# Kernel optimization log

Measured on AMD Instinct MI355X. Metric: run time of the kernel, lower is better.

## Reference

```python
import jax, jax.numpy as jnp
import numpy as np


def setup_inputs() -> dict:
    key = jax.random.key(0)
    k1, k2 = jax.random.split(key)
    z = jax.random.normal(k1, (16, 256, 64, 64), dtype=jnp.float32)  # (t, latent_dim, H, W)
    emb = jax.random.normal(k2, (1024, 256), dtype=jnp.float32)      # (n_codes, latent_dim)
    return {"z": z, "emb": emb}


def reference(z, emb):
    # z: (t, a, b, c) with a == latent_dim; emb: (n_codes, a)
    t, a, b, c = z.shape
    # rearrange 't a b c -> t (b c) a'
    x = z.reshape(t, a, b * c).transpose(0, 2, 1)  # (t, bc, a)
    x2 = jnp.sum(x * x, axis=-1, keepdims=True)          # (t, bc, 1)
    e2 = jnp.sum(emb * emb, axis=-1)                     # (n_codes,)
    d2 = x2 + e2 - 2.0 * jnp.einsum('tna,ka->tnk', x, emb)  # (t, bc, n_codes)
    codes = jnp.argmin(d2, axis=-1)                      # (t, bc)
    return codes.reshape(t, b, c)
```

## Files before the change

### kernel.cpp

```cpp
#include <hip/hip_runtime.h>
#include <hip/hip_bf16.h>

#define TPB 512
#define NCODES 1024
#define DIMS 256
#define PIXB 64
#define DELTA 3.0f
#define CAP 16

typedef __attribute__((ext_vector_type(8))) short bf16x8;
typedef __attribute__((ext_vector_type(4))) float f32x4;

__device__ __forceinline__ void gll16(const void* g, void* l) {
    __builtin_amdgcn_global_load_lds(
        (const __attribute__((address_space(1))) void*)g,
        (__attribute__((address_space(3))) void*)l, 16, 0, 0);
}

__global__ __launch_bounds__(256) void prep_kernel(const float* __restrict__ emb,
                                                   ushort* __restrict__ eb,
                                                   float* __restrict__ e2) {
    const int w = threadIdx.x >> 6;
    const int l = threadIdx.x & 63;
    const int c = blockIdx.x * 4 + w;
    float4 v = *(const float4*)(emb + (size_t)c * DIMS + 4 * l);
    __hip_bfloat16 h0 = __float2bfloat16(v.x), h1 = __float2bfloat16(v.y);
    __hip_bfloat16 h2 = __float2bfloat16(v.z), h3 = __float2bfloat16(v.w);
    ushort4 u;
    u.x = *(ushort*)&h0; u.y = *(ushort*)&h1; u.z = *(ushort*)&h2; u.w = *(ushort*)&h3;
    const int st = (c >> 8) * 8 + (l >> 3);
    const int w8 = (c >> 5) & 7;
    const int cl = c & 31;
    const int j  = (l >> 1) & 3;
    const int e  = (4 * l) & 7;
    *(ushort4*)(eb + (((size_t)(st * 8 + w8) << 10) + (j << 8) + cl * 8 + e)) = u;
    float sq = v.x * v.x + v.y * v.y + v.z * v.z + v.w * v.w;
#pragma unroll
    for (int off = 1; off < 64; off <<= 1) sq += __shfl_xor(sq, off);
    if (l == 0) e2[c] = sq;
}

__global__ __launch_bounds__(TPB, 4) void vq_kernel(const float* __restrict__ z,
                                                    const float* __restrict__ emb,
                                                    const ushort* __restrict__ eb,
                                                    const float* __restrict__ e2g,
                                                    int* __restrict__ out) {
    __shared__ __align__(16) ushort xs2[32 * 64 * 8];
    __shared__ __align__(16) ushort es[2 * 8 * 1024];
    __shared__ float wmin[8 * 64];
    __shared__ float minval[64];
    __shared__ int   cnt[64];
    __shared__ int   cand[64 * CAP];
    __shared__ float scand[64 * CAP];

    const int tid = threadIdx.x;
    const int w   = tid >> 6;
    const int L   = tid & 63;
    const int col = L & 15;
    const int q   = L >> 4;
    const int pixbase = blockIdx.x * PIXB;
    const int t  = pixbase >> 12;
    const int n0 = pixbase & 4095;

#define STAGE(b, st) do {                                                         \
        const ushort* _src = eb + (((size_t)(st) * 8 + w) << 10) + (L << 3);      \
        ushort* _dst = &es[(((b) << 3) + w) * 1024];                              \
        gll16(_src,       _dst);                                                  \
        gll16(_src + 512, _dst + 512);                                            \
    } while (0)

    const float* zbase = z + (((size_t)t * DIMS) << 12) + n0;

#define STAGE_Z(r_, h_) do {                                                      \
        _Pragma("unroll")                                                         \
        for (int i = 0; i < 2; ++i) {                                             \
            const float* _src = zbase                                             \
                + ((size_t)((r_) * 64 + w * 8 + i * 4 + (L >> 4)) << 12)          \
                + ((L & 15) << 2);                                                \
            ushort* _dst = &es[(h_) * 8192 + (w * 2 + i) * 512];                  \
            gll16(_src, _dst);                                                    \
        }                                                                         \
    } while (0)

#define CONVERT(r_, h_) do {                                                      \
        const float* _zs = (const float*)&es[(h_) * 8192];                        \
        _Pragma("unroll")                                                         \
        for (int j = 0; j < 2; ++j) {                                             \
            const int _dl = w * 8 + j * 4;                                        \
            float _a0 = _zs[(_dl + 0) * 64 + L];                                  \
            float _a1 = _zs[(_dl + 1) * 64 + L];                                  \
            float _a2 = _zs[(_dl + 2) * 64 + L];                                  \
            float _a3 = _zs[(_dl + 3) * 64 + L];                                  \
            __hip_bfloat16 _h0 = __float2bfloat16(_a0);                           \
            __hip_bfloat16 _h1 = __float2bfloat16(_a1);                           \
            __hip_bfloat16 _h2 = __float2bfloat16(_a2);                           \
            __hip_bfloat16 _h3 = __float2bfloat16(_a3);                           \
            ushort4 _u;                                                           \
            _u.x = *(ushort*)&_h0; _u.y = *(ushort*)&_h1;                         \
            _u.z = *(ushort*)&_h2; _u.w = *(ushort*)&_h3;                         \
            const int _d0 = (r_) * 64 + _dl;                                      \
            *(ushort4*)&xs2[(size_t)(((_d0 >> 3) * 64 + L) * 8 + (_d0 & 4))] = _u;\
        }                                                                         \
    } while (0)

    STAGE_Z(0, 0);
    STAGE_Z(1, 1);
    if (tid < 64) { minval[tid] = 3.4e38f; cnt[tid] = 0; }
    asm volatile("s_waitcnt vmcnt(2)" ::: "memory");
    CONVERT(0, 0);
    asm volatile("s_waitcnt lgkmcnt(0)" ::: "memory");
    STAGE_Z(2, 0);
    asm volatile("s_waitcnt vmcnt(2)" ::: "memory");
    CONVERT(1, 1);
    asm volatile("s_waitcnt lgkmcnt(0)" ::: "memory");
    STAGE_Z(3, 1);
    asm volatile("s_waitcnt vmcnt(2)" ::: "memory");
    CONVERT(2, 0);
    asm volatile("s_waitcnt lgkmcnt(0)" ::: "memory");
    STAGE(0, 0);
    asm volatile("s_waitcnt vmcnt(2)" ::: "memory");
    CONVERT(3, 1);
    __syncthreads();

#pragma unroll 1
    for (int cc = 0; cc < 4; ++cc) {
        f32x4 acc[2][4];
#pragma unroll
        for (int mt = 0; mt < 2; ++mt)
#pragma unroll
            for (int nt = 0; nt < 4; ++nt) acc[mt][nt] = (f32x4){0.f, 0.f, 0.f, 0.f};

#pragma unroll
        for (int kc = 0; kc < 8; ++kc) {
            const int s = cc * 8 + kc;
            const int b = s & 1;
            if (s < 31) {
                STAGE(b ^ 1, s + 1);
                asm volatile("s_waitcnt vmcnt(2)" ::: "memory");
            } else {
                asm volatile("s_waitcnt vmcnt(0)" ::: "memory");
            }

            bf16x8 af[2], bfr[4];
            const ushort* ws = &es[((b << 3) + w) * 1024 + (q << 8)];
#pragma unroll
            for (int mt = 0; mt < 2; ++mt)
                af[mt] = *(const bf16x8*)(ws + (mt * 16 + col) * 8);
#pragma unroll
            for (int nt = 0; nt < 4; ++nt)
                bfr[nt] = *(const bf16x8*)&xs2[(size_t)(((kc * 4 + q) * 64 + nt * 16 + col) * 8)];
            __builtin_amdgcn_s_setprio(1);
#pragma unroll
            for (int mt = 0; mt < 2; ++mt)
#pragma unroll
                for (int nt = 0; nt < 4; ++nt)
                    acc[mt][nt] = __builtin_amdgcn_mfma_f32_16x16x32_bf16(
                        af[mt], bfr[nt], acc[mt][nt], 0, 0, 0);
            __builtin_amdgcn_s_setprio(0);
        }

        f32x4 e4[2];
#pragma unroll
        for (int mt = 0; mt < 2; ++mt)
            e4[mt] = *(const f32x4*)(e2g + cc * 256 + w * 32 + mt * 16 + q * 4);

#pragma unroll
        for (int nt = 0; nt < 4; ++nt) {
            float m = 3.4e38f;
#pragma unroll
            for (int mt = 0; mt < 2; ++mt)
#pragma unroll
                for (int r = 0; r < 4; ++r) {
                    float s = e4[mt][r] - 2.f * acc[mt][nt][r];
                    m = fminf(m, s);
                }
            m = fminf(m, __shfl_xor(m, 16));
            m = fminf(m, __shfl_xor(m, 32));
            wmin[w * 64 + nt * 16 + col] = m;
        }
        __syncthreads();
        if (tid < 64) {
            float m = minval[tid];
#pragma unroll
            for (int ww = 0; ww < 8; ++ww) m = fminf(m, wmin[ww * 64 + tid]);
            minval[tid] = m;
        }
        __syncthreads();
#pragma unroll
        for (int nt = 0; nt < 4; ++nt) {
            const int px = nt * 16 + col;
            const float thr = minval[px] + DELTA;
#pragma unroll
            for (int mt = 0; mt < 2; ++mt)
#pragma unroll
                for (int r = 0; r < 4; ++r) {
                    float s = e4[mt][r] - 2.f * acc[mt][nt][r];
                    if (s <= thr) {
                        int pos = atomicAdd(&cnt[px], 1);
                        if (pos < CAP) {
                            cand[px * CAP + pos]  = cc * 256 + w * 32 + mt * 16 + q * 4 + r;
                            scand[px * CAP + pos] = s;
                        }
                    }
                }
        }
    }
    __syncthreads();

#pragma unroll 1
    for (int pi = 0; pi < 8; ++pi) {
        const int px = w * 8 + pi;
        const int n  = cnt[px];
        if (n <= CAP) {
            const float thr = minval[px] + DELTA;
            bool surv = (L < n) && (scand[px * CAP + L] <= thr);
            unsigned long long mask = __ballot(surv);
            if (__popcll(mask) == 1) {
                if (L == 0) out[pixbase + px] = cand[px * CAP + (__ffsll(mask) - 1)];
                continue;
            }
            const float* zp = z + (((size_t)t * DIMS + 4 * L) << 12) + n0 + px;
            float x0 = zp[0];
            float x1 = zp[(size_t)1 << 12];
            float x2 = zp[(size_t)2 << 12];
            float x3 = zp[(size_t)3 << 12];
            float bs = 3.4e38f;
            int   bi = 0;
            unsigned long long mm = mask;
            while (mm) {
                int k = __ffsll(mm) - 1; mm &= mm - 1;
                int c = cand[px * CAP + k];
                float4 ev = *(const float4*)(emb + (size_t)c * DIMS + 4 * L);
                float p = x0 * ev.x + x1 * ev.y + x2 * ev.z + x3 * ev.w;
#pragma unroll
                for (int off = 1; off < 64; off <<= 1) p += __shfl_xor(p, off);
                float s = e2g[c] - 2.f * p;
                if (s < bs || (s == bs && c < bi)) { bs = s; bi = c; }
            }
            if (L == 0) out[pixbase + px] = bi;
        } else {
            const float* zp = z + (((size_t)t * DIMS + 4 * L) << 12) + n0 + px;
            float x0 = zp[0];
            float x1 = zp[(size_t)1 << 12];
            float x2 = zp[(size_t)2 << 12];
            float x3 = zp[(size_t)3 << 12];
            float bs = 3.4e38f;
            int   bi = 0;
            for (int c = 0; c < NCODES; ++c) {
                float4 ev = *(const float4*)(emb + (size_t)c * DIMS + 4 * L);
                float p = x0 * ev.x + x1 * ev.y + x2 * ev.z + x3 * ev.w;
#pragma unroll
                for (int off = 1; off < 64; off <<= 1) p += __shfl_xor(p, off);
                float s = e2g[c] - 2.f * p;
                if (s < bs || (s == bs && c < bi)) { bs = s; bi = c; }
            }
            if (L == 0) out[pixbase + px] = bi;
        }
    }
#undef STAGE
#undef STAGE_Z
#undef CONVERT
}

extern "C" void kernel_launch(void* const* d_in, const int* in_sizes, int n_in,
                              void* d_out, int out_size, void* d_ws, size_t ws_size,
                              hipStream_t stream) {
    const float* z   = (const float*)d_in[0];
    const float* emb = (const float*)d_in[1];
    int* out = (int*)d_out;

    ushort* eb = (ushort*)d_ws;
    float*  e2 = (float*)((char*)d_ws + (size_t)NCODES * DIMS * sizeof(ushort));

    prep_kernel<<<256, 256, 0, stream>>>(emb, eb, e2);
    vq_kernel<<<(16 * 64 * 64) / PIXB, TPB, 0, stream>>>(z, emb, eb, e2, out);
}
```

Before: 163.3 us.

## Load codebook fragments directly into registers and shrink LDS for higher occupancy

The codebook tiles are no longer staged through a double-buffered LDS region. Each wave now loads its A fragments straight from global memory into registers, prefetching two k-steps ahead. The z staging shrinks to one 16-byte load per lane per round (eight rounds instead of four), and the epilogue scratch arrays are aliased into a single 16 KB pool, cutting LDS per block. Launch bounds are raised to 6 blocks per CU to exploit the lower LDS footprint. In exchange the kernel takes on more global-load latency exposure and register pressure, which may cause spills under the tighter register budget.

```diff
diff --git a/kernel.cpp b/kernel.cpp
--- a/kernel.cpp
+++ b/kernel.cpp
@@ -40,18 +40,19 @@
     if (l == 0) e2[c] = sq;
 }
 
-__global__ __launch_bounds__(TPB, 4) void vq_kernel(const float* __restrict__ z,
+__global__ __launch_bounds__(TPB, 6) void vq_kernel(const float* __restrict__ z,
                                                     const float* __restrict__ emb,
                                                     const ushort* __restrict__ eb,
                                                     const float* __restrict__ e2g,
                                                     int* __restrict__ out) {
     __shared__ __align__(16) ushort xs2[32 * 64 * 8];
-    __shared__ __align__(16) ushort es[2 * 8 * 1024];
-    __shared__ float wmin[8 * 64];
-    __shared__ float minval[64];
-    __shared__ int   cnt[64];
-    __shared__ int   cand[64 * CAP];
-    __shared__ float scand[64 * CAP];
+    __shared__ __align__(16) char pool[16384];
+
+    float* const wmin   = (float*)pool;
+    float* const minval = (float*)(pool + 2048);
+    int*   const cnt    = (int*)(pool + 2304);
+    int*   const cand   = (int*)(pool + 2560);
+    float* const scand  = (float*)(pool + 6656);
 
     const int tid = threadIdx.x;
     const int w   = tid >> 6;
@@ -62,65 +63,77 @@
     const int t  = pixbase >> 12;
     const int n0 = pixbase & 4095;
 
-#define STAGE(b, st) do {                                                         \
-        const ushort* _src = eb + (((size_t)(st) * 8 + w) << 10) + (L << 3);      \
-        ushort* _dst = &es[(((b) << 3) + w) * 1024];                              \
-        gll16(_src,       _dst);                                                  \
-        gll16(_src + 512, _dst + 512);                                            \
+    const float* zbase = z + (((size_t)t * DIMS) << 12) + n0;
+
+#define STAGE_Z(r_, h_) do {                                                      \
+        const float* _src = zbase                                                 \
+            + ((size_t)((r_) * 32 + w * 4 + (L >> 4)) << 12) + ((L & 15) << 2);   \
+        char* _dst = pool + (h_) * 8192 + (w << 10);                              \
+        gll16(_src, _dst);                                                        \
     } while (0)
 
-    const float* zbase = z + (((size_t)t * DIMS) << 12) + n0;
-
-#define STAGE_Z(r_, h_) do {                                                      \
-        _Pragma("unroll")                                                         \
-        for (int i = 0; i < 2; ++i) {                                             \
-            const float* _src = zbase                                             \
-                + ((size_t)((r_) * 64 + w * 8 + i * 4 + (L >> 4)) << 12)          \
-                + ((L & 15) << 2);                                                \
-            ushort* _dst = &es[(h_) * 8192 + (w * 2 + i) * 512];                  \
-            gll16(_src, _dst);                                                    \
-        }                                                                         \
-    } while (0)
-
 #define CONVERT(r_, h_) do {                                                      \
-        const float* _zs = (const float*)&es[(h_) * 8192];                        \
-        _Pragma("unroll")                                                         \
-        for (int j = 0; j < 2; ++j) {                                             \
-            const int _dl = w * 8 + j * 4;                                        \
-            float _a0 = _zs[(_dl + 0) * 64 + L];                                  \
-            float _a1 = _zs[(_dl + 1) * 64 + L];                                  \
-            float _a2 = _zs[(_dl + 2) * 64 + L];                                  \
-            float _a3 = _zs[(_dl + 3) * 64 + L];                                  \
-            __hip_bfloat16 _h0 = __float2bfloat16(_a0);                           \
-            __hip_bfloat16 _h1 = __float2bfloat16(_a1);                           \
-            __hip_bfloat16 _h2 = __float2bfloat16(_a2);                           \
-            __hip_bfloat16 _h3 = __float2bfloat16(_a3);                           \
-            ushort4 _u;                                                           \
-            _u.x = *(ushort*)&_h0; _u.y = *(ushort*)&_h1;                         \
-            _u.z = *(ushort*)&_h2; _u.w = *(ushort*)&_h3;                         \
-            const int _d0 = (r_) * 64 + _dl;                                      \
-            *(ushort4*)&xs2[(size_t)(((_d0 >> 3) * 64 + L) * 8 + (_d0 & 4))] = _u;\
-        }                                                                         \
+        const float* _zs = (const float*)(pool + (h_) * 8192) + (w << 8);         \
+        float _a0 = _zs[L];                                                       \
+        float _a1 = _zs[64 + L];                                                  \
+        float _a2 = _zs[128 + L];                                                 \
+        float _a3 = _zs[192 + L];                                                 \
+        __hip_bfloat16 _h0 = __float2bfloat16(_a0);                               \
+        __hip_bfloat16 _h1 = __float2bfloat16(_a1);                               \
+        __hip_bfloat16 _h2 = __float2bfloat16(_a2);                               \
+        __hip_bfloat16 _h3 = __float2bfloat16(_a3);                               \
+        ushort4 _u;                                                               \
+        _u.x = *(ushort*)&_h0; _u.y = *(ushort*)&_h1;                             \
+        _u.z = *(ushort*)&_h2; _u.w = *(ushort*)&_h3;                             \
+        const int _g = (r_) * 4 + (w >> 1);                                       \
+        *(ushort4*)&xs2[(size_t)((_g * 64 + L) * 8 + ((w & 1) << 2))] = _u;       \
     } while (0)
 
     STAGE_Z(0, 0);
     STAGE_Z(1, 1);
+    asm volatile("s_waitcnt vmcnt(1)" ::: "memory");
+    CONVERT(0, 0);
+    asm volatile("s_waitcnt lgkmcnt(0)" ::: "memory");
+    STAGE_Z(2, 0);
+    asm volatile("s_waitcnt vmcnt(1)" ::: "memory");
+    CONVERT(1, 1);
+    asm volatile("s_waitcnt lgkmcnt(0)" ::: "memory");
+    STAGE_Z(3, 1);
+    asm volatile("s_waitcnt vmcnt(1)" ::: "memory");
+    CONVERT(2, 0);
+    asm volatile("s_waitcnt lgkmcnt(0)" ::: "memory");
+    STAGE_Z(4, 0);
+    asm volatile("s_waitcnt vmcnt(1)" ::: "memory");
+    CONVERT(3, 1);
+    asm volatile("s_waitcnt lgkmcnt(0)" ::: "memory");
+    STAGE_Z(5, 1);
+    asm volatile("s_waitcnt vmcnt(1)" ::: "memory");
+    CONVERT(4, 0);
+    asm volatile("s_waitcnt lgkmcnt(0)" ::: "memory");
+    STAGE_Z(6, 0);
+    asm volatile("s_waitcnt vmcnt(1)" ::: "memory");
+    CONVERT(5, 1);
+    asm volatile("s_waitcnt lgkmcnt(0)" ::: "memory");
+    STAGE_Z(7, 1);
+    asm volatile("s_waitcnt vmcnt(1)" ::: "memory");
+    CONVERT(6, 0);
+    asm volatile("s_waitcnt lgkmcnt(0)" ::: "memory");
+    asm volatile("s_waitcnt vmcnt(0)" ::: "memory");
+    CONVERT(7, 1);
+
+#define LOADT(a0_, a1_, st_) do {                                                 \
+        const ushort* _et = eb + (((size_t)((st_) * 8 + w)) << 10)                \
+                               + (q << 8) + (col << 3);                           \
+        a0_ = *(const bf16x8*)_et;                                                \
+        a1_ = *(const bf16x8*)(_et + 128);                                        \
+    } while (0)
+
+    bf16x8 pf[2][2];
+    LOADT(pf[0][0], pf[0][1], 0);
+    LOADT(pf[1][0], pf[1][1], 1);
+
+    __syncthreads();
     if (tid < 64) { minval[tid] = 3.4e38f; cnt[tid] = 0; }
-    asm volatile("s_waitcnt vmcnt(2)" ::: "memory");
-    CONVERT(0, 0);
-    asm volatile("s_waitcnt lgkmcnt(0)" ::: "memory");
-    STAGE_Z(2, 0);
-    asm volatile("s_waitcnt vmcnt(2)" ::: "memory");
-    CONVERT(1, 1);
-    asm volatile("s_waitcnt lgkmcnt(0)" ::: "memory");
-    STAGE_Z(3, 1);
-    asm volatile("s_waitcnt vmcnt(2)" ::: "memory");
-    CONVERT(2, 0);
-    asm volatile("s_waitcnt lgkmcnt(0)" ::: "memory");
-    STAGE(0, 0);
-    asm volatile("s_waitcnt vmcnt(2)" ::: "memory");
-    CONVERT(3, 1);
-    __syncthreads();
 
 #pragma unroll 1
     for (int cc = 0; cc < 4; ++cc) {
@@ -133,29 +146,25 @@
 #pragma unroll
         for (int kc = 0; kc < 8; ++kc) {
             const int s = cc * 8 + kc;
-            const int b = s & 1;
-            if (s < 31) {
-                STAGE(b ^ 1, s + 1);
-                asm volatile("s_waitcnt vmcnt(2)" ::: "memory");
-            } else {
-                asm volatile("s_waitcnt vmcnt(0)" ::: "memory");
-            }
-
-            bf16x8 af[2], bfr[4];
-            const ushort* ws = &es[((b << 3) + w) * 1024 + (q << 8)];
-#pragma unroll
-            for (int mt = 0; mt < 2; ++mt)
-                af[mt] = *(const bf16x8*)(ws + (mt * 16 + col) * 8);
+            bf16x8 a0 = pf[kc & 1][0];
+            bf16x8 a1 = pf[kc & 1][1];
+            bf16x8 bfr[4];
 #pragma unroll
             for (int nt = 0; nt < 4; ++nt)
                 bfr[nt] = *(const bf16x8*)&xs2[(size_t)(((kc * 4 + q) * 64 + nt * 16 + col) * 8)];
+            {
+                const int st = (s + 2 < 31) ? s + 2 : 31;
+                LOADT(pf[kc & 1][0], pf[kc & 1][1], st);
+            }
             __builtin_amdgcn_s_setprio(1);
 #pragma unroll
-            for (int mt = 0; mt < 2; ++mt)
-#pragma unroll
-                for (int nt = 0; nt < 4; ++nt)
-                    acc[mt][nt] = __builtin_amdgcn_mfma_f32_16x16x32_bf16(
-                        af[mt], bfr[nt], acc[mt][nt], 0, 0, 0);
+            for (int nt = 0; nt < 4; ++nt)
+                acc[0][nt] = __builtin_amdgcn_mfma_f32_16x16x32_bf16(
+                    a0, bfr[nt], acc[0][nt], 0, 0, 0);
+#pragma unroll
+            for (int nt = 0; nt < 4; ++nt)
+                acc[1][nt] = __builtin_amdgcn_mfma_f32_16x16x32_bf16(
+                    a1, bfr[nt], acc[1][nt], 0, 0, 0);
             __builtin_amdgcn_s_setprio(0);
         }
 
@@ -257,9 +266,9 @@
             if (L == 0) out[pixbase + px] = bi;
         }
     }
-#undef STAGE
 #undef STAGE_Z
 #undef CONVERT
+#undef LOADT
 }
 
 extern "C" void kernel_launch(void* const* d_in, const int* in_sizes, int n_in,
```

Result: slower. 239.9 us (+46.9%).
